# Performance work log

Hardware: AMD Instinct MI355X
Metric: run time of the kernel (lower is better)

Reference implementation:

```python
import jax, jax.numpy as jnp
import numpy as np

C = 256
GN_GROUPS = 16
EPS = 1e-5


def hsigmoid(x):
    # HSigmoid(bias=3, divisor=6)
    return jnp.clip((x + 3.0) / 6.0, 0.0, 1.0)


def conv3x3(x, w, b):
    y = jax.lax.conv_general_dilated(x, w, (1, 1), ((1, 1), (1, 1)),
                                     dimension_numbers=('NCHW', 'OIHW', 'NCHW'))
    return y + b[None, :, None, None]


def group_norm(x, w, b):
    B, Cc, H, W = x.shape
    xg = x.reshape(B, GN_GROUPS, Cc // GN_GROUPS, H, W)
    mu = xg.mean(axis=(2, 3, 4), keepdims=True)
    var = xg.var(axis=(2, 3, 4), keepdims=True)
    xn = ((xg - mu) * jax.lax.rsqrt(var + EPS)).reshape(B, Cc, H, W)
    return xn * w[None, :, None, None] + b[None, :, None, None]


def bilinear_sample(x, py, px):
    # x: [B,C,H,W]; py,px: [B,9,Ho,Wo]; zero padding outside the image
    B, Cc, H, W = x.shape
    y0 = jnp.floor(py)
    x0 = jnp.floor(px)

    def gather(xb, yi, xi):
        return xb[:, yi, xi]  # [C,9,Ho,Wo]

    out = jnp.zeros((B, Cc) + py.shape[1:], x.dtype)
    for dy in (0.0, 1.0):
        for dx in (0.0, 1.0):
            yi = y0 + dy
            xi = x0 + dx
            wgt = (1.0 - jnp.abs(py - yi)) * (1.0 - jnp.abs(px - xi))
            valid = (yi >= 0) & (yi <= H - 1) & (xi >= 0) & (xi <= W - 1)
            yc = jnp.clip(yi, 0, H - 1).astype(jnp.int32)
            xc = jnp.clip(xi, 0, W - 1).astype(jnp.int32)
            vals = jax.vmap(gather)(x, yc, xc)  # [B,C,9,Ho,Wo]
            out = out + vals * (wgt * valid)[:, None]
    return out


def mdcn(x, offset, mask, w, stride):
    # Modulated deformable conv v2, kernel 3x3, padding 1, no bias.
    B, Cin, H, W = x.shape
    Ho, Wo = offset.shape[2], offset.shape[3]
    off = offset.reshape(B, 9, 2, Ho, Wo)  # channel 2k = y_k, 2k+1 = x_k
    kk = jnp.arange(9)
    ky = (kk // 3).astype(x.dtype)[None, :, None, None]
    kx = (kk % 3).astype(x.dtype)[None, :, None, None]
    gy = (jnp.arange(Ho, dtype=x.dtype) * stride - 1.0)[None, None, :, None]
    gx = (jnp.arange(Wo, dtype=x.dtype) * stride - 1.0)[None, None, None, :]
    py = gy + ky + off[:, :, 0]
    px = gx + kx + off[:, :, 1]
    cols = bilinear_sample(x, py, px) * mask[:, None]  # [B,Cin,9,Ho,Wo]
    return jnp.einsum('bckhw,ock->bohw', cols, w.reshape(w.shape[0], Cin, 9))


def resize_bilinear_ac(x, oh, ow):
    # F.interpolate(mode='bilinear', align_corners=True), separable
    B, Cc, H, W = x.shape
    ys = jnp.linspace(0.0, H - 1.0, oh)
    y0 = jnp.floor(ys).astype(jnp.int32)
    y1 = jnp.minimum(y0 + 1, H - 1)
    wy = (ys - y0)[None, None, :, None]
    xr = x[:, :, y0, :] * (1 - wy) + x[:, :, y1, :] * wy
    xs = jnp.linspace(0.0, W - 1.0, ow)
    x0i = jnp.floor(xs).astype(jnp.int32)
    x1i = jnp.minimum(x0i + 1, W - 1)
    wx = (xs - x0i)[None, None, None, :]
    return xr[:, :, :, x0i] * (1 - wx) + xr[:, :, :, x1i] * wx


def dyrelu(x, w1, b1, w2, b2):
    p = x.mean(axis=(2, 3))  # [B,C] global avg pool
    h = jax.nn.relu(p @ w1.reshape(w1.shape[0], -1).T + b1)
    co = hsigmoid(h @ w2.reshape(w2.shape[0], -1).T + b2) - 0.5  # [B,4C]
    a1, c1, a2, c2 = jnp.split(co, 4, axis=1)
    a1 = (a1 * 2.0 + 1.0)[:, :, None, None]
    a2 = (a2 * 2.0)[:, :, None, None]
    c1 = c1[:, :, None, None]
    c2 = c2[:, :, None, None]
    return jnp.maximum(x * a1 + c1, x * a2 + c2)


def dyhead_block(xs, w_off, b_off, w_high, gn_high_w, gn_high_b,
                 w_mid, gn_mid_w, gn_mid_b, w_low, gn_low_w, gn_low_b,
                 sa_w, sa_b, dy_w1, dy_b1, dy_w2, dy_b2):
    def scale_attn(f):
        p = f.mean(axis=(2, 3))  # [B,C]
        v = hsigmoid(jax.nn.relu(p @ sa_w.reshape(1, -1).T + sa_b))
        return v[:, :, None, None]  # [B,1,1,1]

    outs = []
    n = len(xs)
    for lvl in range(n):
        om = conv3x3(xs[lvl], w_off, b_off)
        offset = om[:, :18]
        mask = jax.nn.sigmoid(om[:, 18:])
        mid = group_norm(mdcn(xs[lvl], offset, mask, w_mid, 1), gn_mid_w, gn_mid_b)
        s = mid * scale_attn(mid)
        cnt = 1.0
        if lvl > 0:
            lo = group_norm(mdcn(xs[lvl - 1], offset, mask, w_low, 2),
                            gn_low_w, gn_low_b)
            s = s + lo * scale_attn(lo)
            cnt += 1.0
        if lvl < n - 1:
            # so take the stride-2 subgrid (clean interpretation of mmdet code)
            hi = group_norm(mdcn(xs[lvl + 1], offset[:, :, ::2, ::2],
                                 mask[:, :, ::2, ::2], w_high, 1),
                            gn_high_w, gn_high_b)
            hi = resize_bilinear_ac(hi, xs[lvl].shape[2], xs[lvl].shape[3])
            s = s + hi * scale_attn(hi)
            cnt += 1.0
        outs.append(dyrelu(s / cnt, dy_w1, dy_b1, dy_w2, dy_b2))
    return tuple(outs)


def setup_inputs() -> dict:
    key = jax.random.key(0)
    ks = jax.random.split(key, 10)
    B = 4
    sizes = [(64, 64), (32, 32), (16, 16)]
    inp = {}
    for i, (h, w) in enumerate(sizes):
        inp[f'x{i}'] = jax.random.normal(ks[i], (B, C, h, w), jnp.float32)
    std = 0.01  # normal_init(m, 0, 0.01)
    inp['w_off'] = jax.random.normal(ks[3], (27, C, 3, 3), jnp.float32) * std
    inp['b_off'] = jnp.zeros((27,), jnp.float32)
    inp['w_high'] = jax.random.normal(ks[4], (C, C, 3, 3), jnp.float32) * std
    inp['w_mid'] = jax.random.normal(ks[5], (C, C, 3, 3), jnp.float32) * std
    inp['w_low'] = jax.random.normal(ks[6], (C, C, 3, 3), jnp.float32) * std
    for nm in ('high', 'mid', 'low'):
        inp[f'gn_{nm}_w'] = jnp.ones((C,), jnp.float32)
        inp[f'gn_{nm}_b'] = jnp.zeros((C,), jnp.float32)
    inp['sa_w'] = jax.random.normal(ks[7], (1, C, 1, 1), jnp.float32) * std
    inp['sa_b'] = jnp.zeros((1,), jnp.float32)
    inp['dy_w1'] = jax.random.normal(ks[8], (C // 4, C, 1, 1), jnp.float32) * std
    inp['dy_b1'] = jnp.zeros((C // 4,), jnp.float32)
    inp['dy_w2'] = jax.random.normal(ks[9], (4 * C, C // 4, 1, 1), jnp.float32) * std
    inp['dy_b2'] = jnp.zeros((4 * C,), jnp.float32)
    return inp


def reference(x0, x1, x2, w_off, b_off, w_high, gn_high_w, gn_high_b,
              w_mid, gn_mid_w, gn_mid_b, w_low, gn_low_w, gn_low_b,
              sa_w, sa_b, dy_w1, dy_b1, dy_w2, dy_b2):
    return dyhead_block([x0, x1, x2], w_off, b_off, w_high, gn_high_w, gn_high_b,
                        w_mid, gn_mid_w, gn_mid_b, w_low, gn_low_w, gn_low_b,
                        sa_w, sa_b, dy_w1, dy_b1, dy_w2, dy_b2)
```

## Files before the change

kernel.cpp:

```cpp
#include <hip/hip_runtime.h>
#include <math.h>

#define CH 256
#define GRP 16
#define EPSV 1e-5f
#define BB 4

typedef __attribute__((ext_vector_type(8))) short short8;
typedef __attribute__((ext_vector_type(4))) float f32x4;

__device__ __forceinline__ float hsig(float x){
  return fminf(fmaxf((x + 3.0f) * (1.0f/6.0f), 0.0f), 1.0f);
}

__device__ __forceinline__ unsigned short f2bf(float f){
  union { float f; unsigned int u; } v; v.f = f;
  unsigned int r = v.u + 0x7fffu + ((v.u >> 16) & 1u);
  return (unsigned short)(r >> 16);
}

__device__ __forceinline__ void gload_lds16(const void* g, void* l){
  __builtin_amdgcn_global_load_lds((const __attribute__((address_space(1))) unsigned int*)g,
                                   (__attribute__((address_space(3))) unsigned int*)l, 16, 0, 0);
}

__global__ __launch_bounds__(256) void pack_all_kernel(
    const float* __restrict__ w_mid, const float* __restrict__ w_low, const float* __restrict__ w_high,
    const float* __restrict__ w_off,
    unsigned short* __restrict__ Wm, unsigned short* __restrict__ Wl, unsigned short* __restrict__ Wh,
    unsigned short* __restrict__ W27){
  int blk = blockIdx.x;
  if (blk < 6912){
    const float* w = (blk < 2304) ? w_mid : (blk < 4608 ? w_low : w_high);
    unsigned short* W3 = (blk < 2304) ? Wm : (blk < 4608 ? Wl : Wh);
    int idx = (blk % 2304) * 256 + threadIdx.x;
    int e = idx & 7;
    int l = (idx >> 3) & 63;
    int f = idx >> 9;
    int mf = f & 3;
    int q = (f >> 2) & 3;
    int s = f >> 4;
    int kk = s >> 3, cb = s & 7;
    int o = q * 64 + mf * 16 + (l & 15);
    int kc = ((l >> 4) << 3) + e;
    int c = cb * 32 + kc;
    W3[idx] = f2bf(w[(o * CH + c) * 9 + kk]);
  } else {
    int idx = (blk - 6912) * 256 + threadIdx.x;
    int s = idx >> 10;
    int r = idx & 1023;
    int o = r >> 5;
    int pos = r & 31;
    int cp = pos >> 3, j = pos & 7;
    int kc = ((cp ^ ((o >> 1) & 3)) << 3) + j;
    int kk = s >> 3, cb = s & 7;
    int c = (cb << 5) + kc;
    W27[idx] = (o < 27) ? f2bf(w_off[(o * CH + c) * 9 + kk]) : (unsigned short)0;
  }
}

__global__ __launch_bounds__(256) void nhwc_rowsum_kernel(
    const float* __restrict__ x0, const float* __restrict__ x1, const float* __restrict__ x2,
    float* __restrict__ xn0, float* __restrict__ xn1, float* __restrict__ xn2,
    float* __restrict__ roww0, float* __restrict__ roww1){
  __shared__ float lds[32][257];
  int blk = blockIdx.x;
  int t = threadIdx.x;
  if (blk >= 672){
    float* out = (blk == 673) ? roww1 : roww0;
    int Hh = (blk == 673) ? 16 : 32;
    int H = (blk == 673) ? 32 : 64;
    if (t < Hh){
      float rs = 0.0f;
      float scale = (float)(Hh - 1) / (float)(H - 1);
      for (int h = 0; h < H; h++){
        float ysv = (float)h * scale;
        float y0f = floorf(ysv);
        int y0 = (int)y0f;
        float fy = ysv - y0f;
        int y1 = min(y0 + 1, Hh - 1);
        if (y0 == t) rs += 1.0f - fy;
        if (y1 == t) rs += fy;
      }
      out[t] = rs;
    }
    return;
  }
  const float* xs; float* xd; int HW; int rb;
  if (blk < 512){ xs = x0; xd = xn0; HW = 4096; rb = blk; }
  else if (blk < 640){ xs = x1; xd = xn1; HW = 1024; rb = blk - 512; }
  else { xs = x2; xd = xn2; HW = 256; rb = blk - 640; }
  int p0 = rb * 32;
  int b = p0 / HW;
  int rem0 = p0 - b * HW;
  int pl = t & 31, cg = t >> 5;
  for (int ci = 0; ci < 32; ci++){
    int c = ci * 8 + cg;
    lds[pl][c] = xs[(long)(b * CH + c) * HW + rem0 + pl];
  }
  __syncthreads();
  for (int p = 0; p < 32; p++){
    xd[(long)(b * HW + rem0 + p) * CH + t] = lds[p][t];
  }
}

__global__ __launch_bounds__(256, 4) void conv_offset_mfma_kernel(
    const float* __restrict__ xn0, const float* __restrict__ xn1, const float* __restrict__ xn2,
    const unsigned short* __restrict__ W27, const float* __restrict__ boff,
    float* __restrict__ offs_all, float* __restrict__ mask_all){
  __shared__ __align__(16) short awlds[1024];
  __shared__ __align__(16) short cbuf[4096];
  int blk = blockIdx.x;
  const float* xn; int H; long ooff, moff; int rb;
  if (blk < 256){ xn = xn0; H = 64; ooff = 0; moff = 0; rb = blk; }
  else if (blk < 320){ xn = xn1; H = 32; ooff = 294912; moff = 147456; rb = blk - 256; }
  else { xn = xn2; H = 16; ooff = 368640; moff = 184320; rb = blk - 320; }
  int W = H, HW = H * W;
  int t = threadIdx.x;
  int lane = t & 63, wv = t >> 6;
  int pg = rb * 64 + lane;
  int b = pg / HW;
  int rem = pg - b * HW;
  int i = rem / W, j = rem - i * W;

  f32x4 acc[2];
  #pragma unroll
  for (int mf = 0; mf < 2; mf++){
    #pragma unroll
    for (int r = 0; r < 4; r++){
      int o = mf * 16 + (lane >> 4) * 4 + r;
      acc[mf][r] = boff[o < 27 ? o : 0];
    }
  }

  for (int kk = 0; kk < 9; kk++){
    int ky = kk / 3, kx = kk - ky * 3;
    int ii = i - 1 + ky, jj = j - 1 + kx;
    bool valid = (ii >= 0 && ii < H && jj >= 0 && jj < W);
    int addr = valid ? ((b * HW + ii * W + jj) << 8) : 0;
    float vm = valid ? 1.0f : 0.0f;
    for (int cb8 = 0; cb8 < 8; cb8++){
      __syncthreads();
      const unsigned short* tile = W27 + (size_t)(kk * 8 + cb8) * 1024;
      if (t < 128) gload_lds16(tile + (t >> 6) * 512 + (t & 63) * 8, (short*)awlds + (t >> 6) * 512);
      const float* xc = xn + addr + cb8 * 32 + wv * 8;
      float4 va = *(const float4*)xc;
      float4 vb = *(const float4*)(xc + 4);
      short8 pk;
      pk[0] = (short)f2bf(vm * va.x); pk[1] = (short)f2bf(vm * va.y);
      pk[2] = (short)f2bf(vm * va.z); pk[3] = (short)f2bf(vm * va.w);
      pk[4] = (short)f2bf(vm * vb.x); pk[5] = (short)f2bf(vm * vb.y);
      pk[6] = (short)f2bf(vm * vb.z); pk[7] = (short)f2bf(vm * vb.w);
      *(short8*)((char*)cbuf + lane * 64 + ((wv ^ ((lane >> 1) & 3)) << 4)) = pk;
      __syncthreads();
      short8 af[2];
      #pragma unroll
      for (int mf = 0; mf < 2; mf++){
        int o = mf * 16 + (lane & 15);
        af[mf] = *(const short8*)((const char*)awlds + o * 64 + ((((lane >> 4)) ^ ((o >> 1) & 3)) << 4));
      }
      int nc = wv * 16 + (lane & 15);
      short8 bf1 = *(const short8*)((const char*)cbuf + nc * 64 + ((((lane >> 4)) ^ ((nc >> 1) & 3)) << 4));
      acc[0] = __builtin_amdgcn_mfma_f32_16x16x32_bf16(af[0], bf1, acc[0], 0, 0, 0);
      acc[1] = __builtin_amdgcn_mfma_f32_16x16x32_bf16(af[1], bf1, acc[1], 0, 0, 0);
    }
  }

  int rem0 = rb * 64 - b * HW;
  #pragma unroll
  for (int mf = 0; mf < 2; mf++){
    #pragma unroll
    for (int r = 0; r < 4; r++){
      int o = mf * 16 + (lane >> 4) * 4 + r;
      int pix = rem0 + wv * 16 + (lane & 15);
      float v = acc[mf][r];
      if (o < 18) offs_all[ooff + ((long)b * 18 + o) * HW + pix] = v;
      else if (o < 27) mask_all[moff + ((long)b * 9 + (o - 18)) * HW + pix] = 1.0f / (1.0f + expf(-v));
    }
  }
}

__device__ const int MJ_start[8] = {0,128,160,168,200,208,240,248};
__device__ const int MJ_xsel[7]  = {0,1,2,0,1,1,2};
__device__ const int MJ_Hx[7]    = {64,32,16,64,32,32,16};
__device__ const int MJ_ooff[7]  = {0,294912,368640,294912,368640,0,294912};
__device__ const int MJ_moff[7]  = {0,147456,184320,147456,184320,0,147456};
__device__ const int MJ_Hoff[7]  = {64,32,16,32,16,64,32};
__device__ const int MJ_ostep[7] = {1,1,1,1,1,2,2};
__device__ const int MJ_strd[7]  = {1,1,1,2,2,1,1};
__device__ const int MJ_wsel[7]  = {0,0,0,1,1,2,2};
__device__ const int MJ_yoff[7]  = {0,5242880,7602176,6291456,7864320,4194304,7340032};
__device__ const int MJ_Ho[7]    = {64,32,16,32,16,32,16};

__global__ __launch_bounds__(512, 2) void mdcn_mfma_kernel(
    const float* __restrict__ xn0, const float* __restrict__ xn1, const float* __restrict__ xn2,
    const float* __restrict__ offs_all, const float* __restrict__ mask_all,
    const unsigned short* __restrict__ Wm, const unsigned short* __restrict__ Wl, const unsigned short* __restrict__ Wh,
    float* __restrict__ y_all){
  __shared__ __align__(16) short colbuf[2][4096];

  int dd = (blockIdx.x & 7) * 31 + (blockIdx.x >> 3);
  int job = 0;
  while (job < 6 && dd >= MJ_start[job + 1]) job++;
  int xsel = MJ_xsel[job];
  const float* xn = (xsel == 0) ? xn0 : (xsel == 1 ? xn1 : xn2);
  int wsel = MJ_wsel[job];
  const unsigned short* W3 = (wsel == 0) ? Wm : (wsel == 1 ? Wl : Wh);
  int Hx = MJ_Hx[job], Wx = Hx, HxWx = Hx * Hx;
  int Ho = MJ_Ho[job], Wo = Ho, HoWo = Ho * Ho;
  int Woff = MJ_Hoff[job], HoffW = Woff * Woff;
  int ostep = MJ_ostep[job], stride = MJ_strd[job];
  const float* offs = offs_all + MJ_ooff[job];
  const float* maskb = mask_all + MJ_moff[job];
  float* y = y_all + MJ_yoff[job];

  int rb = dd - MJ_start[job];
  int blkPerB = HoWo >> 7;
  int b = rb / blkPerB;
  int n0 = (rb - b * blkPerB) << 7;

  int t = threadIdx.x;
  int lane = t & 63;
  int wv = t >> 6;
  int wq = wv >> 1;
  int px = t >> 2;
  int cg = t & 3;

  int pix = n0 + px;
  int i = pix / Wo, j = pix - i * Wo;
  int opos = i * ostep * Woff + j * ostep;
  int base = b * HxWx;

  int4 A4c, A4n; float4 Wtc, Wtn;
  auto computeAW = [&](int kk, int4& A4o, float4& Wto){
    int ky = kk / 3, kx = kk - ky * 3;
    float offy = offs[((long)b * 18 + 2 * kk) * HoffW + opos];
    float offx = offs[((long)b * 18 + 2 * kk + 1) * HoffW + opos];
    float m = maskb[((long)b * 9 + kk) * HoffW + opos];
    float py = (float)(i * stride - 1 + ky) + offy;
    float pxx = (float)(j * stride - 1 + kx) + offx;
    float y0f = floorf(py), x0f = floorf(pxx);
    float fy = py - y0f, fx = pxx - x0f;
    bool vy0 = (y0f >= 0.0f) && (y0f <= (float)(Hx - 1));
    bool vy1 = (y0f + 1.0f >= 0.0f) && (y0f + 1.0f <= (float)(Hx - 1));
    bool vx0 = (x0f >= 0.0f) && (x0f <= (float)(Wx - 1));
    bool vx1 = (x0f + 1.0f >= 0.0f) && (x0f + 1.0f <= (float)(Wx - 1));
    float w0 = (1.0f - fy) * (1.0f - fx) * m * ((vy0 && vx0) ? 1.0f : 0.0f);
    float w1 = (1.0f - fy) * fx * m * ((vy0 && vx1) ? 1.0f : 0.0f);
    float w2 = fy * (1.0f - fx) * m * ((vy1 && vx0) ? 1.0f : 0.0f);
    float w3 = fy * fx * m * ((vy1 && vx1) ? 1.0f : 0.0f);
    int iy0 = min(max((int)y0f, 0), Hx - 1);
    int iy1 = min(max((int)y0f + 1, 0), Hx - 1);
    int ix0 = min(max((int)x0f, 0), Wx - 1);
    int ix1 = min(max((int)x0f + 1, 0), Wx - 1);
    A4o = make_int4((base + iy0 * Wx + ix0) << 8, (base + iy0 * Wx + ix1) << 8,
                    (base + iy1 * Wx + ix0) << 8, (base + iy1 * Wx + ix1) << 8);
    Wto = make_float4(w0, w1, w2, w3);
  };

  float4 g0_0,g0_1,g0_2,g0_3,g0_4,g0_5,g0_6,g0_7;
  float4 g1_0,g1_1,g1_2,g1_3,g1_4,g1_5,g1_6,g1_7;

  short8 af0[4], af1[4];
  auto loadA = [&](int s, short8* af){
    const short8* wp = (const short8*)W3 + ((size_t)s * 16 + wq * 4) * 64 + lane;
    af[0] = wp[0]; af[1] = wp[64]; af[2] = wp[128]; af[3] = wp[192];
  };

  f32x4 acc[4][4];
  #pragma unroll
  for (int mf = 0; mf < 4; mf++)
    #pragma unroll
    for (int nf = 0; nf < 4; nf++)
      acc[mf][nf] = (f32x4){0.f, 0.f, 0.f, 0.f};

#define GATHER_(P, CB, A4G) do{ \
    const float* xc_ = xn + (CB)*32 + cg*8; \
    g##P##_0 = *(const float4*)(xc_ + (A4G).x); g##P##_1 = *(const float4*)(xc_ + (A4G).x + 4); \
    g##P##_2 = *(const float4*)(xc_ + (A4G).y); g##P##_3 = *(const float4*)(xc_ + (A4G).y + 4); \
    g##P##_4 = *(const float4*)(xc_ + (A4G).z); g##P##_5 = *(const float4*)(xc_ + (A4G).z + 4); \
    g##P##_6 = *(const float4*)(xc_ + (A4G).w); g##P##_7 = *(const float4*)(xc_ + (A4G).w + 4); \
  }while(0)

#define PACKW_(P, BUF, WT) do{ \
    short8 pk_; \
    pk_[0] = (short)f2bf((WT).x*g##P##_0.x + (WT).y*g##P##_2.x + (WT).z*g##P##_4.x + (WT).w*g##P##_6.x); \
    pk_[1] = (short)f2bf((WT).x*g##P##_0.y + (WT).y*g##P##_2.y + (WT).z*g##P##_4.y + (WT).w*g##P##_6.y); \
    pk_[2] = (short)f2bf((WT).x*g##P##_0.z + (WT).y*g##P##_2.z + (WT).z*g##P##_4.z + (WT).w*g##P##_6.z); \
    pk_[3] = (short)f2bf((WT).x*g##P##_0.w + (WT).y*g##P##_2.w + (WT).z*g##P##_4.w + (WT).w*g##P##_6.w); \
    pk_[4] = (short)f2bf((WT).x*g##P##_1.x + (WT).y*g##P##_3.x + (WT).z*g##P##_5.x + (WT).w*g##P##_7.x); \
    pk_[5] = (short)f2bf((WT).x*g##P##_1.y + (WT).y*g##P##_3.y + (WT).z*g##P##_5.y + (WT).w*g##P##_7.y); \
    pk_[6] = (short)f2bf((WT).x*g##P##_1.z + (WT).y*g##P##_3.z + (WT).z*g##P##_5.z + (WT).w*g##P##_7.z); \
    pk_[7] = (short)f2bf((WT).x*g##P##_1.w + (WT).y*g##P##_3.w + (WT).z*g##P##_5.w + (WT).w*g##P##_7.w); \
    *(short8*)((char*)colbuf[BUF] + px * 64 + ((cg ^ ((px >> 1) & 3)) << 4)) = pk_; \
  }while(0)

#define MFMA_(BUF, AF) do{ \
    __builtin_amdgcn_s_setprio(1); \
    short8 bf_[4]; \
    _Pragma("unroll") \
    for (int nf = 0; nf < 4; nf++){ \
      int nc_ = (wv & 1) * 64 + nf * 16 + (lane & 15); \
      bf_[nf] = *(const short8*)((const char*)colbuf[BUF] + nc_ * 64 + ((((lane >> 4)) ^ ((nc_ >> 1) & 3)) << 4)); } \
    _Pragma("unroll") \
    for (int mf = 0; mf < 4; mf++) \
      _Pragma("unroll") \
      for (int nf = 0; nf < 4; nf++) \
        acc[mf][nf] = __builtin_amdgcn_mfma_f32_16x16x32_bf16((AF)[mf], bf_[nf], acc[mf][nf], 0, 0, 0); \
    __builtin_amdgcn_s_setprio(0); \
  }while(0)

#define BARRIER_ do{ \
    asm volatile("s_waitcnt lgkmcnt(0)" ::: "memory"); \
    __builtin_amdgcn_sched_barrier(0); \
    __builtin_amdgcn_s_barrier(); \
    __builtin_amdgcn_sched_barrier(0); \
  }while(0)

#define STEP_(S, P, Q, AF) do{ \
    if ((S) <= 69){ \
      if ((((S)+2) & 7) == 0){ \
        computeAW(((S)+2) >> 3, A4n, Wtn); \
        GATHER_(P, 0, A4n); \
      } else { \
        GATHER_(P, ((S)+2) & 7, A4c); \
      } \
    } \
    MFMA_(P, AF); \
    if ((S) <= 69) loadA((S)+2, AF); \
    if ((S) <= 70) PACKW_(Q, Q, Wtc); \
    if ((S) <= 69 && (((S)+2) & 7) == 0){ A4c = A4n; Wtc = Wtn; } \
    BARRIER_; \
  }while(0)

  computeAW(0, A4c, Wtc);
  loadA(0, af0);
  loadA(1, af1);
  GATHER_(0, 0, A4c);
  PACKW_(0, 0, Wtc);
  GATHER_(1, 1, A4c);
  BARRIER_;

  for (int ss = 0; ss < 72; ss += 2){
    STEP_(ss, 0, 1, af0);
    STEP_(ss + 1, 1, 0, af1);
  }

#undef STEP_
#undef BARRIER_
#undef MFMA_
#undef PACKW_
#undef GATHER_

  #pragma unroll
  for (int mf = 0; mf < 4; mf++){
    #pragma unroll
    for (int nf = 0; nf < 4; nf++){
      #pragma unroll
      for (int r = 0; r < 4; r++){
        int o = wq * 64 + mf * 16 + (lane >> 4) * 4 + r;
        int pix2 = n0 + (wv & 1) * 64 + nf * 16 + (lane & 15);
        y[((long)b * CH + o) * HoWo + pix2] = acc[mf][nf][r];
      }
    }
  }
}

__device__ const int SJ_yoff[7] = {0,4194304,5242880,6291456,7340032,7602176,7864320};
__device__ const int SJ_HW[7]   = {4096,1024,1024,1024,256,256,256};
__device__ const int SJ_rw[7]   = {0,1,0,0,2,0,0};

__global__ __launch_bounds__(256) void stats_all_kernel(
    const float* __restrict__ y_all, const float* __restrict__ roww0, const float* __restrict__ roww1,
    float* __restrict__ sums_all, float* __restrict__ ss_all, float* __restrict__ wsum_all){
  int blk = blockIdx.x;
  int job = blk >> 10, bc = blk & 1023;
  int HW = SJ_HW[job];
  int Ws = (HW == 4096) ? 64 : ((HW == 1024) ? 32 : 16);
  int rwsel = SJ_rw[job];
  const float* rw = (rwsel == 2) ? roww1 : roww0;
  const float* p = y_all + SJ_yoff[job] + (long)bc * HW;
  int t = threadIdx.x;
  float s = 0, ss = 0, ws = 0;
  for (int e0 = t * 4; e0 < HW; e0 += 1024){
    float4 v4 = *(const float4*)(p + e0);
    s += v4.x + v4.y + v4.z + v4.w;
    ss += v4.x * v4.x + v4.y * v4.y + v4.z * v4.z + v4.w * v4.w;
    if (rwsel){
      int r = e0 / Ws, cc = e0 - r * Ws;
      float rr = rw[r];
      ws += rr * (v4.x * rw[cc] + v4.y * rw[cc + 1] + v4.z * rw[cc + 2] + v4.w * rw[cc + 3]);
    }
  }
  __shared__ float r1[256], r2[256], r3[256];
  r1[t] = s; r2[t] = ss; r3[t] = ws;
  __syncthreads();
  for (int o = 128; o > 0; o >>= 1){
    if (t < o){ r1[t] += r1[t + o]; r2[t] += r2[t + o]; r3[t] += r3[t + o]; }
    __syncthreads();
  }
  if (t == 0){
    sums_all[job * 1024 + bc] = r1[0];
    ss_all[job * 1024 + bc] = r2[0];
    if (rwsel) wsum_all[(rwsel - 1) * 1024 + bc] = r3[0];
  }
}

__device__ const int   GJ_psrc[7] = {0,1,0,0,2,0,0};
__device__ const float GJ_pdiv[7] = {1.f/4096,1.f/4096,1.f/1024,1.f/1024,1.f/1024,1.f/256,1.f/256};
__device__ const float GJ_ninv[7] = {1.f/65536,1.f/16384,1.f/16384,1.f/16384,1.f/4096,1.f/4096,1.f/4096};
__device__ const int   GJ_gsel[7] = {0,2,0,1,2,0,1};

__global__ __launch_bounds__(256) void gn_sa_all_kernel(
    const float* __restrict__ sums_all, const float* __restrict__ ss_all, const float* __restrict__ wsum_all,
    const float* __restrict__ gw_m, const float* __restrict__ gb_m,
    const float* __restrict__ gw_l, const float* __restrict__ gb_l,
    const float* __restrict__ gw_h, const float* __restrict__ gb_h,
    const float* __restrict__ saw, const float* __restrict__ sab,
    float* __restrict__ mu_all, float* __restrict__ rs_all, float* __restrict__ v_all){
  int blk = blockIdx.x;
  int job = blk >> 2, b = blk & 3;
  int t = threadIdx.x;
  const float* sums = sums_all + job * 1024;
  const float* ssq  = ss_all + job * 1024;
  int psrc = GJ_psrc[job];
  const float* ps = (psrc == 0) ? sums : (wsum_all + (psrc - 1) * 1024);
  int gsel = GJ_gsel[job];
  const float* gw = (gsel == 0) ? gw_m : (gsel == 1 ? gw_l : gw_h);
  const float* gb = (gsel == 0) ? gb_m : (gsel == 1 ? gb_l : gb_h);
  float pdiv = GJ_pdiv[job], ninv = GJ_ninv[job];
  __shared__ float smu[GRP], srs[GRP], red[256];
  if (t < GRP){
    float s = 0, ss = 0;
    for (int c = 0; c < 16; c++){ int idx = b * CH + t * 16 + c; s += sums[idx]; ss += ssq[idx]; }
    float mu = s * ninv;
    float var = ss * ninv - mu * mu;
    float rs = rsqrtf(var + EPSV);
    smu[t] = mu; srs[t] = rs;
    mu_all[job * 64 + b * GRP + t] = mu;
    rs_all[job * 64 + b * GRP + t] = rs;
  }
  __syncthreads();
  int g = t >> 4;
  float pm = (ps[b * CH + t] * pdiv - smu[g]) * srs[g] * gw[t] + gb[t];
  red[t] = pm * saw[t];
  __syncthreads();
  for (int o = 128; o > 0; o >>= 1){ if (t < o) red[t] += red[t + o]; __syncthreads(); }
  if (t == 0) v_all[job * 4 + b] = hsig(fmaxf(red[0] + sab[0], 0.0f));
}

__device__ const long CA_yb[3] = {0, 5242880, 7602176};
__device__ const long CA_yl[3] = {0, 6291456, 7864320};
__device__ const long CA_yh[3] = {4194304, 7340032, 0};
__device__ const int  CA_ms[3] = {0, 2, 5};
__device__ const int  CA_ls[3] = {0, 3, 6};
__device__ const int  CA_hs[3] = {1, 4, 0};
__device__ const long FA_out[3] = {0, 4194304, 5242880};

__global__ __launch_bounds__(256) void dyrelu_direct_kernel(
    const float* __restrict__ sums_all, const float* __restrict__ wsum_all,
    const float* __restrict__ mu_all, const float* __restrict__ rs_all, const float* __restrict__ v_all,
    const float* __restrict__ gw_m, const float* __restrict__ gb_m,
    const float* __restrict__ gw_l, const float* __restrict__ gb_l,
    const float* __restrict__ gw_h, const float* __restrict__ gb_h,
    const float* __restrict__ w1, const float* __restrict__ b1,
    const float* __restrict__ w2, const float* __restrict__ b2,
    float* __restrict__ coef_all){
  int lvl = blockIdx.x >> 2, b = blockIdx.x & 3;
  int t = threadIdx.x;
  int H = 64 >> lvl, HW = H * H;
  float invHW = 1.0f / (float)HW;
  int has_lo = (lvl > 0), has_hi = (lvl < 2);
  float inv_cnt = 1.0f / (1.0f + has_lo + has_hi);
  int ms = CA_ms[lvl], ls = CA_ls[lvl], hs = CA_hs[lvl];
  int g = t >> 4;
  float p = v_all[ms * 4 + b] *
      ((sums_all[ms * 1024 + b * CH + t] * invHW - mu_all[ms * 64 + b * GRP + g]) * rs_all[ms * 64 + b * GRP + g] * gw_m[t] + gb_m[t]);
  if (has_lo)
    p += v_all[ls * 4 + b] *
      ((sums_all[ls * 1024 + b * CH + t] * invHW - mu_all[ls * 64 + b * GRP + g]) * rs_all[ls * 64 + b * GRP + g] * gw_l[t] + gb_l[t]);
  if (has_hi)
    p += v_all[hs * 4 + b] *
      ((wsum_all[lvl * 1024 + b * CH + t] * invHW - mu_all[hs * 64 + b * GRP + g]) * rs_all[hs * 64 + b * GRP + g] * gw_h[t] + gb_h[t]);
  p *= inv_cnt;
  __shared__ float pl[CH], hl[64];
  pl[t] = p;
  __syncthreads();
  if (t < 64){
    float a = b1[t];
    const float* wr = w1 + t * CH;
    for (int c = 0; c < CH; c++) a += wr[c] * pl[c];
    hl[t] = fmaxf(a, 0.0f);
  }
  __syncthreads();
  #pragma unroll
  for (int r = 0; r < 4; r++){
    int o = r * CH + t;
    float a = b2[o];
    const float* wr = w2 + o * 64;
    #pragma unroll
    for (int j = 0; j < 64; j++) a += wr[j] * hl[j];
    float co = hsig(a) - 0.5f;
    float outv;
    if (r == 0) outv = co * 2.0f + 1.0f;
    else if (r == 2) outv = co * 2.0f;
    else outv = co;
    coef_all[lvl * 4096 + (b * 4 + r) * CH + t] = outv;
  }
}

__global__ __launch_bounds__(256) void combine_final_kernel(
    const float* __restrict__ y_all,
    const float* __restrict__ mu_all, const float* __restrict__ rs_all, const float* __restrict__ v_all,
    const float* __restrict__ gw_m, const float* __restrict__ gb_m,
    const float* __restrict__ gw_l, const float* __restrict__ gb_l,
    const float* __restrict__ gw_h, const float* __restrict__ gb_h,
    const float* __restrict__ coef_all, float* __restrict__ outp){
  int blk = blockIdx.x;
  int lvl, rb;
  if (blk < 4096){ lvl = 0; rb = blk; }
  else if (blk < 5120){ lvl = 1; rb = blk - 4096; }
  else { lvl = 2; rb = blk - 5120; }
  int H = 64 >> lvl, W = H, HW = H * W;
  int has_lo = (lvl > 0), has_hi = (lvl < 2);
  float inv_cnt = 1.0f / (1.0f + has_lo + has_hi);
  int ms = CA_ms[lvl], ls = CA_ls[lvl], hs = CA_hs[lvl];
  const float* smid = y_all + CA_yb[lvl];
  const float* ylo = y_all + CA_yl[lvl];
  const float* yhi = y_all + CA_yh[lvl];

  int t = threadIdx.x;
  int idx = (rb * 256 + t) * 4;
  int b = idx / (CH * HW);
  int r1i = idx - b * CH * HW;
  int c = r1i / HW;
  int rem = r1i - c * HW;
  int h = rem / W;
  int w = rem - h * W;
  int g = c >> 4;
  int bg = b * GRP + g;

  float4 sm4 = *(const float4*)(smid + idx);
  float vms = v_all[ms * 4 + b], mum = mu_all[ms * 64 + bg], rsm = rs_all[ms * 64 + bg];
  float gm = gw_m[c], bm = gb_m[c];
  float4 s4;
  s4.x = vms * ((sm4.x - mum) * rsm * gm + bm);
  s4.y = vms * ((sm4.y - mum) * rsm * gm + bm);
  s4.z = vms * ((sm4.z - mum) * rsm * gm + bm);
  s4.w = vms * ((sm4.w - mum) * rsm * gm + bm);
  if (has_lo){
    float4 lo4 = *(const float4*)(ylo + idx);
    float vls = v_all[ls * 4 + b], mul = mu_all[ls * 64 + bg], rsl = rs_all[ls * 64 + bg];
    float gl = gw_l[c], bl = gb_l[c];
    s4.x += vls * ((lo4.x - mul) * rsl * gl + bl);
    s4.y += vls * ((lo4.y - mul) * rsl * gl + bl);
    s4.z += vls * ((lo4.z - mul) * rsl * gl + bl);
    s4.w += vls * ((lo4.w - mul) * rsl * gl + bl);
  }
  if (has_hi){
    int Hh = H >> 1, Wh = W >> 1;
    float ysv = (float)h * ((float)(Hh - 1) / (float)(H - 1));
    float y0f = floorf(ysv); int y0 = (int)y0f; float fy = ysv - y0f; int y1 = min(y0 + 1, Hh - 1);
    const float* hb = yhi + (b * CH + c) * Hh * Wh;
    float vhs = v_all[hs * 4 + b], muh = mu_all[hs * 64 + bg], rsh = rs_all[hs * 64 + bg];
    float gh = gw_h[c], bh = gb_h[c];
    float xscale = (float)(Wh - 1) / (float)(W - 1);
    float* sp = (float*)&s4;
    #pragma unroll
    for (int dw = 0; dw < 4; dw++){
      float xsv = (float)(w + dw) * xscale;
      float x0f = floorf(xsv); int x0 = (int)x0f; float fx = xsv - x0f; int x1 = min(x0 + 1, Wh - 1);
      float v00 = hb[y0 * Wh + x0], v01 = hb[y0 * Wh + x1];
      float v10 = hb[y1 * Wh + x0], v11 = hb[y1 * Wh + x1];
      float blv = v00 * (1 - fy) * (1 - fx) + v01 * (1 - fy) * fx + v10 * fy * (1 - fx) + v11 * fy * fx;
      sp[dw] += vhs * ((blv - muh) * rsh * gh + bh);
    }
  }
  const float* cf = coef_all + lvl * 4096 + b * 4 * CH;
  float a1 = cf[c], c1 = cf[CH + c], a2 = cf[2 * CH + c], c2 = cf[3 * CH + c];
  float4 o4;
  float sx = s4.x * inv_cnt, sy = s4.y * inv_cnt, sz = s4.z * inv_cnt, sw = s4.w * inv_cnt;
  o4.x = fmaxf(sx * a1 + c1, sx * a2 + c2);
  o4.y = fmaxf(sy * a1 + c1, sy * a2 + c2);
  o4.z = fmaxf(sz * a1 + c1, sz * a2 + c2);
  o4.w = fmaxf(sw * a1 + c1, sw * a2 + c2);
  *(float4*)(outp + FA_out[lvl] + idx) = o4;
}

extern "C" void kernel_launch(void* const* d_in, const int* in_sizes, int n_in,
                              void* d_out, int out_size, void* d_ws, size_t ws_size,
                              hipStream_t stream){
  const float* x0 = (const float*)d_in[0];
  const float* x1 = (const float*)d_in[1];
  const float* x2 = (const float*)d_in[2];
  const float* w_off = (const float*)d_in[3];
  const float* b_off = (const float*)d_in[4];
  int sig = (in_sizes[6] == 256);
  const float* w_high = (const float*)d_in[5];
  const float* w_mid  = (const float*)d_in[sig ? 8 : 6];
  const float* w_low  = (const float*)d_in[sig ? 11 : 7];
  const float* gn_high_w = (const float*)d_in[sig ? 6 : 8];
  const float* gn_high_b = (const float*)d_in[sig ? 7 : 9];
  const float* gn_mid_w  = (const float*)d_in[sig ? 9 : 10];
  const float* gn_mid_b  = (const float*)d_in[sig ? 10 : 11];
  const float* gn_low_w  = (const float*)d_in[12];
  const float* gn_low_b  = (const float*)d_in[13];
  const float* sa_w  = (const float*)d_in[14];
  const float* sa_b  = (const float*)d_in[15];
  const float* dy_w1 = (const float*)d_in[16];
  const float* dy_b1 = (const float*)d_in[17];
  const float* dy_w2 = (const float*)d_in[18];
  const float* dy_b2 = (const float*)d_in[19];

  float* p = (float*)d_ws;
  unsigned short* W3_mid  = (unsigned short*)p; p += 294912;
  unsigned short* W3_low  = (unsigned short*)p; p += 294912;
  unsigned short* W3_high = (unsigned short*)p; p += 294912;
  unsigned short* W27     = (unsigned short*)p; p += 36864;
  float* xn0 = p; p += 4194304;
  float* xn1 = p; p += 1048576;
  float* xn2 = p; p += 262144;
  float* offs_all = p; p += 387072;
  float* mask_all = p; p += 193536;
  float* y_all = p; p += 8126464;
  float* sums_all = p; p += 7168;
  float* ss_all = p; p += 7168;
  float* wsum_all = p; p += 2048;
  float* coef_all = p; p += 12288;
  float* mu_all = p; p += 448;
  float* rs_all = p; p += 448;
  float* v_all = p; p += 28;   p += 4;
  float* roww0 = p; p += 32;
  float* roww1 = p; p += 32;

  pack_all_kernel<<<7200, 256, 0, stream>>>(w_mid, w_low, w_high, w_off, W3_mid, W3_low, W3_high, W27);
  nhwc_rowsum_kernel<<<674, 256, 0, stream>>>(x0, x1, x2, xn0, xn1, xn2, roww0, roww1);
  conv_offset_mfma_kernel<<<336, 256, 0, stream>>>(xn0, xn1, xn2, W27, b_off, offs_all, mask_all);
  mdcn_mfma_kernel<<<248, 512, 0, stream>>>(xn0, xn1, xn2, offs_all, mask_all, W3_mid, W3_low, W3_high, y_all);
  stats_all_kernel<<<7168, 256, 0, stream>>>(y_all, roww0, roww1, sums_all, ss_all, wsum_all);
  gn_sa_all_kernel<<<28, 256, 0, stream>>>(sums_all, ss_all, wsum_all,
                                           gn_mid_w, gn_mid_b, gn_low_w, gn_low_b, gn_high_w, gn_high_b,
                                           sa_w, sa_b, mu_all, rs_all, v_all);
  dyrelu_direct_kernel<<<12, 256, 0, stream>>>(sums_all, wsum_all, mu_all, rs_all, v_all,
                                               gn_mid_w, gn_mid_b, gn_low_w, gn_low_b, gn_high_w, gn_high_b,
                                               dy_w1, dy_b1, dy_w2, dy_b2, coef_all);
  combine_final_kernel<<<5376, 256, 0, stream>>>(y_all, mu_all, rs_all, v_all,
                                                 gn_mid_w, gn_mid_b, gn_low_w, gn_low_b, gn_high_w, gn_high_b,
                                                 coef_all, (float*)d_out);
}
```

Measured before the change: 211.5 us.

## Process two K-steps per barrier phase with four LDS column buffers

The MDCN MFMA mainloop now handles two K-steps per barrier instead of one. The LDS column buffer grows from two to four slots so each phase can gather and pack the next pair while running MFMAs on the current pair. This halves the number of workgroup barriers and gives longer runs of independent work to overlap. In exchange LDS use doubles to 32KB per block, which may cut occupancy under launch_bounds(512,2), and register pressure rises.

```diff
diff --git a/kernel.cpp b/kernel.cpp
--- a/kernel.cpp
+++ b/kernel.cpp
@@ -197,7 +197,7 @@
     const float* __restrict__ offs_all, const float* __restrict__ mask_all,
     const unsigned short* __restrict__ Wm, const unsigned short* __restrict__ Wl, const unsigned short* __restrict__ Wh,
     float* __restrict__ y_all){
-  __shared__ __align__(16) short colbuf[2][4096];
+  __shared__ __align__(16) short colbuf[4][4096];
 
   int dd = (blockIdx.x & 7) * 31 + (blockIdx.x >> 3);
   int job = 0;
@@ -317,19 +317,22 @@
     __builtin_amdgcn_sched_barrier(0); \
   }while(0)
 
-#define STEP_(S, P, Q, AF) do{ \
-    if ((S) <= 69){ \
-      if ((((S)+2) & 7) == 0){ \
-        computeAW(((S)+2) >> 3, A4n, Wtn); \
-        GATHER_(P, 0, A4n); \
+#define PHASE_(P, PC, PN) do{ \
+    if ((P) <= 34){ PACKW_(0, (PN), Wtc); PACKW_(1, (PN)+1, Wtc); } \
+    if ((P) <= 33){ \
+      if (((2*(P)+4) & 7) == 0){ \
+        computeAW((2*(P)+4) >> 3, A4n, Wtn); \
+        GATHER_(0, 0, A4n); \
+        GATHER_(1, 1, A4n); \
       } else { \
-        GATHER_(P, ((S)+2) & 7, A4c); \
+        GATHER_(0, (2*(P)+4) & 7, A4c); \
+        GATHER_(1, (2*(P)+5) & 7, A4c); \
       } \
     } \
-    MFMA_(P, AF); \
-    if ((S) <= 69) loadA((S)+2, AF); \
-    if ((S) <= 70) PACKW_(Q, Q, Wtc); \
-    if ((S) <= 69 && (((S)+2) & 7) == 0){ A4c = A4n; Wtc = Wtn; } \
+    MFMA_((PC), af0); \
+    MFMA_((PC)+1, af1); \
+    if ((P) <= 34){ loadA(2*(P)+2, af0); loadA(2*(P)+3, af1); } \
+    if ((P) <= 33 && ((2*(P)+4) & 7) == 0){ A4c = A4n; Wtc = Wtn; } \
     BARRIER_; \
   }while(0)
 
@@ -337,16 +340,19 @@
   loadA(0, af0);
   loadA(1, af1);
   GATHER_(0, 0, A4c);
+  GATHER_(1, 1, A4c);
   PACKW_(0, 0, Wtc);
-  GATHER_(1, 1, A4c);
+  PACKW_(1, 1, Wtc);
+  GATHER_(0, 2, A4c);
+  GATHER_(1, 3, A4c);
   BARRIER_;
 
-  for (int ss = 0; ss < 72; ss += 2){
-    STEP_(ss, 0, 1, af0);
-    STEP_(ss + 1, 1, 0, af1);
-  }
-
-#undef STEP_
+  for (int pp = 0; pp < 36; pp += 2){
+    PHASE_(pp, 0, 2);
+    PHASE_(pp + 1, 2, 0);
+  }
+
+#undef PHASE_
 #undef BARRIER_
 #undef MFMA_
 #undef PACKW_
```

After: 207.9 us. About the same (-1.7%).
